# Optimization experiments

Hardware: AMD Instinct MI355X
Metric: run time of the kernel (lower is better)

The kernel has to match this reference:

```python
import jax, jax.numpy as jnp
import numpy as np

EPS = 1e-9
NUM_HEADS = 16
D = 1024      # input_dim == hidden_dim
B, S = 2, 2048


def layer_norm(x, scale, shift):
    mu = x.mean(axis=-1, keepdims=True)
    # torch std is unbiased (ddof=1); eps added to std, not variance
    std = jnp.std(x, axis=-1, ddof=1, keepdims=True)
    return scale * (x - mu) / (std + EPS) + shift


def setup_inputs() -> dict:
    key = jax.random.key(0)
    ks = jax.random.split(key, 18)
    d, h = D, D
    w = lambda k, sh: jax.random.normal(k, sh, dtype=jnp.float32) * 0.02
    return {
        "inputs": jax.random.normal(ks[0], (B, S, d), dtype=jnp.float32),
        "ln1_scale": jax.random.normal(ks[1], (d,), dtype=jnp.float32),
        "ln1_shift": jax.random.normal(ks[2], (d,), dtype=jnp.float32),
        "Wq": w(ks[3], (d, h)), "bq": jnp.zeros((h,), jnp.float32),
        "Wk": w(ks[4], (d, h)), "bk": jnp.zeros((h,), jnp.float32),
        "Wv": w(ks[5], (d, h)), "bv": jnp.zeros((h,), jnp.float32),
        "Wo": w(ks[6], (h, d)), "bo": jnp.zeros((d,), jnp.float32),
        "W1": w(ks[7], (d, 4 * d)), "b1": jnp.zeros((4 * d,), jnp.float32),
        "W2": w(ks[8], (4 * d, d)), "b2": jnp.zeros((d,), jnp.float32),
        "ln2_scale": jax.random.normal(ks[9], (d,), dtype=jnp.float32),
        "ln2_shift": jax.random.normal(ks[10], (d,), dtype=jnp.float32),
    }


def mhsa(x, Wq, bq, Wk, bk, Wv, bv, Wo, bo):
    b, s, d = x.shape
    nh, dh = NUM_HEADS, D // NUM_HEADS
    q = (x @ Wq + bq).reshape(b, s, nh, dh).transpose(0, 2, 1, 3)  # b h s d
    k = (x @ Wk + bk).reshape(b, s, nh, dh).transpose(0, 2, 1, 3)
    v = (x @ Wv + bv).reshape(b, s, nh, dh).transpose(0, 2, 1, 3)
    scores = jnp.einsum("bhqd,bhkd->bhqk", q, k) / jnp.sqrt(jnp.float32(dh))
    causal = jnp.triu(jnp.ones((s, s), dtype=bool), k=1)  # mask above diagonal
    scores = jnp.where(causal, -jnp.inf, scores)
    p = jax.nn.softmax(scores, axis=-1)
    p = jnp.where(jnp.isnan(p), 0.0, p)  # NaN-fill as in original
    out = jnp.einsum("bhqk,bhkd->bhqd", p, v)
    out = out.transpose(0, 2, 1, 3).reshape(b, s, nh * dh)
    return out @ Wo + bo


def reference(inputs, ln1_scale, ln1_shift, Wq, bq, Wk, bk, Wv, bv, Wo, bo,
              W1, b1, W2, b2, ln2_scale, ln2_shift):
    o1 = layer_norm(inputs, ln1_scale, ln1_shift)
    o1 = mhsa(o1, Wq, bq, Wk, bk, Wv, bv, Wo, bo) + inputs
    o2 = layer_norm(o1, ln2_scale, ln2_shift)
    # NOTE: original adds the residual from the *normalized* tensor, not o1
    ffn = jax.nn.relu(o2 @ W1 + b1) @ W2 + b2
    return ffn + o2
```

## Files before the change

### kernel.cpp

```cpp
#include <hip/hip_runtime.h>
#include <hip/hip_bf16.h>
#include <math.h>

#define BB 2
#define SS 2048
#define DD 1024
#define HH 16
#define DH 64
#define NROW (BB*SS)
#define FFN (4*DD)

typedef __attribute__((ext_vector_type(8))) __bf16 bf16x8;
typedef __attribute__((ext_vector_type(4))) __bf16 bf16x4;
typedef __attribute__((ext_vector_type(4))) float f32x4;

#define QSCALE 0.18033688011112042f

__device__ __forceinline__ ushort f2b(float f) {
    union { float f; uint32_t u; } x; x.f = f;
    uint32_t r = x.u + 0x7FFF + ((x.u >> 16) & 1);
    return (ushort)(r >> 16);
}
__device__ __forceinline__ float b2f(ushort u) {
    union { uint32_t u; float f; } x; x.u = (uint32_t)u << 16;
    return x.f;
}

__global__ __launch_bounds__(256)
void ln_kernel(const float* __restrict__ x, const float* __restrict__ scale,
               const float* __restrict__ shift, ushort* __restrict__ y) {
    int row = blockIdx.x;
    const float* xr = x + (size_t)row * DD;
    ushort* yr = y + (size_t)row * DD;
    int t = threadIdx.x;
    float v[4];
    float s = 0.f, ss = 0.f;
#pragma unroll
    for (int i = 0; i < 4; ++i) {
        v[i] = xr[t + 256 * i];
        s += v[i];
        ss += v[i] * v[i];
    }
#pragma unroll
    for (int off = 32; off; off >>= 1) {
        s  += __shfl_xor(s, off);
        ss += __shfl_xor(ss, off);
    }
    __shared__ float red[8];
    int w = t >> 6;
    if ((t & 63) == 0) { red[w] = s; red[w + 4] = ss; }
    __syncthreads();
    float st  = red[0] + red[1] + red[2] + red[3];
    float sst = red[4] + red[5] + red[6] + red[7];
    float mu = st * (1.f / DD);
    float var = (sst - DD * mu * mu) * (1.f / (DD - 1));
    var = fmaxf(var, 0.f);
    float inv = 1.f / (sqrtf(var) + 1e-9f);
#pragma unroll
    for (int i = 0; i < 4; ++i) {
        int c = t + 256 * i;
        yr[c] = f2b(scale[c] * (v[i] - mu) * inv + shift[c]);
    }
}

__global__ __launch_bounds__(256)
void ln_res_kernel(const ushort* __restrict__ xa, const float* __restrict__ xb,
                   const float* __restrict__ scale, const float* __restrict__ shift,
                   ushort* __restrict__ yb) {
    int row = blockIdx.x;
    const ushort* ar = xa + (size_t)row * DD;
    const float* br = xb + (size_t)row * DD;
    ushort* ybr = yb + (size_t)row * DD;
    int t = threadIdx.x;
    float v[4];
    float s = 0.f, ss = 0.f;
#pragma unroll
    for (int i = 0; i < 4; ++i) {
        int c = t + 256 * i;
        v[i] = b2f(ar[c]) + br[c];
        s += v[i];
        ss += v[i] * v[i];
    }
#pragma unroll
    for (int off = 32; off; off >>= 1) {
        s  += __shfl_xor(s, off);
        ss += __shfl_xor(ss, off);
    }
    __shared__ float red[8];
    int w = t >> 6;
    if ((t & 63) == 0) { red[w] = s; red[w + 4] = ss; }
    __syncthreads();
    float st  = red[0] + red[1] + red[2] + red[3];
    float sst = red[4] + red[5] + red[6] + red[7];
    float mu = st * (1.f / DD);
    float var = (sst - DD * mu * mu) * (1.f / (DD - 1));
    var = fmaxf(var, 0.f);
    float inv = 1.f / (sqrtf(var) + 1e-9f);
#pragma unroll
    for (int i = 0; i < 4; ++i) {
        int c = t + 256 * i;
        ybr[c] = f2b(scale[c] * (v[i] - mu) * inv + shift[c]);
    }
}

__global__ __launch_bounds__(256)
void transpose_bf16_kernel(const float* __restrict__ W, ushort* __restrict__ Wt,
                           int K, int N) {
    __shared__ ushort tile[32][33];
    int tx = threadIdx.x & 31;
    int ty = threadIdx.x >> 5;
    int n0 = blockIdx.x * 32;
    int k0 = blockIdx.y * 32;
#pragma unroll
    for (int i = 0; i < 32; i += 8)
        tile[ty + i][tx] = f2b(W[(size_t)(k0 + ty + i) * N + n0 + tx]);
    __syncthreads();
#pragma unroll
    for (int i = 0; i < 32; i += 8)
        Wt[(size_t)(n0 + ty + i) * K + k0 + tx] = tile[tx][ty + i];
}

__global__ __launch_bounds__(256)
void transpose4_bf16_kernel(const float* __restrict__ W0, const float* __restrict__ W1,
                            const float* __restrict__ W2, const float* __restrict__ W3,
                            ushort* __restrict__ Wt) {
    __shared__ ushort tile[32][33];
    int z = blockIdx.z;
    const float* W = z == 0 ? W0 : (z == 1 ? W1 : (z == 2 ? W2 : W3));
    ushort* dst = Wt + (size_t)z * DD * DD;
    int tx = threadIdx.x & 31;
    int ty = threadIdx.x >> 5;
    int n0 = blockIdx.x * 32;
    int k0 = blockIdx.y * 32;
#pragma unroll
    for (int i = 0; i < 32; i += 8)
        tile[ty + i][tx] = f2b(W[(size_t)(k0 + ty + i) * DD + n0 + tx]);
    __syncthreads();
#pragma unroll
    for (int i = 0; i < 32; i += 8)
        dst[(size_t)(n0 + ty + i) * DD + k0 + tx] = tile[tx][ty + i];
}

__global__ __launch_bounds__(256)
void reduce_wo_kernel(const float* __restrict__ p0, const float* __restrict__ p1,
                      const float* __restrict__ bias, ushort* __restrict__ yb) {
    int i = (blockIdx.x * 256 + threadIdx.x) * 4;
    float4 a = *reinterpret_cast<const float4*>(p0 + i);
    float4 b = *reinterpret_cast<const float4*>(p1 + i);
    int c = i & (DD - 1);
    float4 bs = *reinterpret_cast<const float4*>(bias + c);
    ushort4 o;
    o.x = f2b(a.x + b.x + bs.x);
    o.y = f2b(a.y + b.y + bs.y);
    o.z = f2b(a.z + b.z + bs.z);
    o.w = f2b(a.w + b.w + bs.w);
    *reinterpret_cast<ushort4*>(yb + i) = o;
}

__global__ __launch_bounds__(256)
void reduce_ffn2_kernel(const float* __restrict__ p0, const float* __restrict__ p1,
                        const float* __restrict__ bias, const ushort* __restrict__ res,
                        float* __restrict__ out) {
    int i = (blockIdx.x * 256 + threadIdx.x) * 4;
    float4 a = *reinterpret_cast<const float4*>(p0 + i);
    float4 b = *reinterpret_cast<const float4*>(p1 + i);
    ushort4 r = *reinterpret_cast<const ushort4*>(res + i);
    int c = i & (DD - 1);
    float4 bs = *reinterpret_cast<const float4*>(bias + c);
    float4 o;
    o.x = a.x + b.x + bs.x + b2f(r.x);
    o.y = a.y + b.y + bs.y + b2f(r.y);
    o.z = a.z + b.z + bs.z + b2f(r.z);
    o.w = a.w + b.w + bs.w + b2f(r.w);
    *reinterpret_cast<float4*>(out + i) = o;
}

#define GBM 128
#define GBK 32

template <int MODE, bool BF16_OUT, int DEPTH, int BN>
__global__ __launch_bounds__(512)
void gemm_bf16_kernel(const ushort* __restrict__ A, const ushort* __restrict__ Wt,
                      const float* __restrict__ bias, const ushort* __restrict__ addsrc,
                      void* __restrict__ Cout, int M, int N, int K, int lda,
                      const float* __restrict__ bias2, const float* __restrict__ bias3,
                      void* __restrict__ out2, void* __restrict__ out3) {
    __shared__ ushort As[DEPTH][GBM * GBK];
    __shared__ ushort Bs[DEPTH][BN * GBK];
    constexpr int NF = BN / 64;

    int tid = threadIdx.x;
    int lane = tid & 63;
    int wid = tid >> 6;
    int wr = wid >> 2, wc = wid & 3;

    int gx = gridDim.x;
    int nwg = gx * gridDim.y;
    int orig = blockIdx.y * gx + blockIdx.x;
    int q8 = nwg >> 3;
    int swz = (orig & 7) * q8 + (orig >> 3);
    int bx = swz % gx, by = swz / gx;

    int brow = by * GBM;
    int bcol = bx * BN;
    size_t koff = (size_t)blockIdx.z * K;

    int lrow = lane & 15;
    int kgrp = lane >> 4;

    f32x4 acc[4][NF] = {};

    auto stage = [&](int buf, int k0) {
        {
            int row = tid >> 2;
            int gran = (tid & 3) ^ ((row >> 1) & 3);
            const char* ga = (const char*)A +
                ((size_t)(brow + row) * lda + koff + k0) * 2 + gran * 16;
            __builtin_amdgcn_global_load_lds(
                (const __attribute__((address_space(1))) uint32_t*)ga,
                (__attribute__((address_space(3))) uint32_t*)(&As[buf][0] + (wid * 16) * GBK),
                16, 0, 0);
        }
#pragma unroll
        for (int i = 0; i < BN / 128; ++i) {
            int idx = i * 512 + tid;
            int row = idx >> 2;
            int gran = (idx & 3) ^ ((row >> 1) & 3);
            const char* gb = (const char*)Wt +
                ((size_t)(bcol + row) * lda + koff + k0) * 2 + gran * 16;
            __builtin_amdgcn_global_load_lds(
                (const __attribute__((address_space(1))) uint32_t*)gb,
                (__attribute__((address_space(3))) uint32_t*)(&Bs[buf][0] + (i * 128 + wid * 16) * GBK),
                16, 0, 0);
        }
    };

    int nk = K / GBK;
    constexpr int PRE = DEPTH - 1;
#pragma unroll
    for (int s = 0; s < PRE; ++s)
        if (s < nk) stage(s, s * GBK);

    int cur = 0, stg = PRE;
    for (int t = 0; t < nk; ++t) {
        __builtin_amdgcn_sched_barrier(0);
        int rem = nk - 1 - t;
        if constexpr (DEPTH == 5 && BN == 128) {
            if (rem >= 3)      asm volatile("s_waitcnt vmcnt(6)" ::: "memory");
            else if (rem == 2) asm volatile("s_waitcnt vmcnt(4)" ::: "memory");
            else if (rem == 1) asm volatile("s_waitcnt vmcnt(2)" ::: "memory");
            else               asm volatile("s_waitcnt vmcnt(0)" ::: "memory");
        } else if constexpr (DEPTH == 3 && BN == 128) {
            if (rem >= 1)      asm volatile("s_waitcnt vmcnt(2)" ::: "memory");
            else               asm volatile("s_waitcnt vmcnt(0)" ::: "memory");
        } else if constexpr (DEPTH == 3 && BN == 256) {
            if (rem >= 1)      asm volatile("s_waitcnt vmcnt(3)" ::: "memory");
            else               asm volatile("s_waitcnt vmcnt(0)" ::: "memory");
        } else {
            asm volatile("s_waitcnt vmcnt(0)" ::: "memory");
        }
        asm volatile("s_barrier" ::: "memory");
        if (t + PRE < nk) stage(stg, (t + PRE) * GBK);

        bf16x8 afrag[4], bfrag[NF];
#pragma unroll
        for (int mi = 0; mi < 4; ++mi) {
            int row = wr * 64 + mi * 16 + lrow;
            int gran = kgrp ^ ((row >> 1) & 3);
            afrag[mi] = *(const bf16x8*)((const char*)&As[cur][0] + row * 64 + gran * 16);
        }
#pragma unroll
        for (int ni = 0; ni < NF; ++ni) {
            int row = wc * (BN / 4) + ni * 16 + lrow;
            int gran = kgrp ^ ((row >> 1) & 3);
            bfrag[ni] = *(const bf16x8*)((const char*)&Bs[cur][0] + row * 64 + gran * 16);
        }
#pragma unroll
        for (int mi = 0; mi < 4; ++mi)
#pragma unroll
            for (int ni = 0; ni < NF; ++ni)
                acc[mi][ni] = __builtin_amdgcn_mfma_f32_16x16x32_bf16(
                    afrag[mi], bfrag[ni], acc[mi][ni], 0, 0, 0);

        cur = (cur == DEPTH - 1) ? 0 : cur + 1;
        stg = (stg == DEPTH - 1) ? 0 : stg + 1;
    }

    if (MODE == 3) {
        int which = bcol >> 10;
        const float* bs = which == 0 ? bias : (which == 1 ? bias2 : bias3);
#pragma unroll
        for (int ni = 0; ni < NF; ++ni) {
            int col = bcol + wc * (BN / 4) + ni * 16 + lrow;
            int lcol = col & 1023;
            float bsv = bs[lcol];
#pragma unroll
            for (int mi = 0; mi < 4; ++mi) {
                f32x4 a = acc[mi][ni];
#pragma unroll
                for (int j = 0; j < 4; ++j) {
                    int row = brow + wr * 64 + mi * 16 + kgrp * 4 + j;
                    float val = a[j] + bsv;
                    if (which == 2) {
                        size_t idx = (size_t)(row >> 11) * ((size_t)DD * SS)
                                   + (size_t)lcol * SS + (row & (SS - 1));
                        ((ushort*)out3)[idx] = f2b(val);
                    } else if (which == 0) {
                        ((ushort*)Cout)[(size_t)row * DD + lcol] = f2b(val * QSCALE);
                    } else {
                        ((ushort*)out2)[(size_t)row * DD + lcol] = f2b(val);
                    }
                }
            }
        }
        return;
    }

    if (MODE == 4) {
        float* dst = (float*)Cout + (size_t)blockIdx.z * ((size_t)M * N);
#pragma unroll
        for (int ni = 0; ni < NF; ++ni) {
            int col = bcol + wc * (BN / 4) + ni * 16 + lrow;
#pragma unroll
            for (int mi = 0; mi < 4; ++mi) {
                f32x4 a = acc[mi][ni];
#pragma unroll
                for (int j = 0; j < 4; ++j) {
                    int row = brow + wr * 64 + mi * 16 + kgrp * 4 + j;
                    dst[(size_t)row * N + col] = a[j];
                }
            }
        }
        return;
    }

#pragma unroll
    for (int ni = 0; ni < NF; ++ni) {
        int col = bcol + wc * (BN / 4) + ni * 16 + lrow;
        float bsv = bias[col];
#pragma unroll
        for (int mi = 0; mi < 4; ++mi) {
            f32x4 a = acc[mi][ni];
#pragma unroll
            for (int j = 0; j < 4; ++j) {
                int row = brow + wr * 64 + mi * 16 + kgrp * 4 + j;
                float val = a[j] + bsv;
                if (MODE == 1) val = fmaxf(val, 0.f);
                if (BF16_OUT)
                    ((ushort*)Cout)[(size_t)row * N + col] = f2b(val);
                else
                    ((float*)Cout)[(size_t)row * N + col] = val;
            }
        }
    }
}

__global__ __launch_bounds__(256)
void attn_mfma_kernel(const ushort* __restrict__ Qg, const ushort* __restrict__ Kg,
                      const ushort* __restrict__ Vtg, ushort* __restrict__ Og) {
    __shared__ ushort Qs[64 * 64];
    __shared__ ushort Ks[2][64 * 64];
    __shared__ ushort Vs[2][64 * 64];

    int tid = threadIdx.x;
    int lane = tid & 63;
    int wid = tid >> 6;
    int bh = blockIdx.x;
    int b = bh >> 4, h = bh & 15;
    int y = blockIdx.y;
    int jj = y >> 3, kk = y & 7;
    int qt = jj * 8 + ((jj & 1) ? 7 - kk : kk);
    int q0 = qt * 64;

    const ushort* Qbase = Qg + ((size_t)(b * SS + q0)) * DD + h * DH;
    const ushort* Kbase = Kg + ((size_t)(b * SS)) * DD + h * DH;
    const ushort* Vbase = Vtg + (size_t)bh * DH * SS;

    int r0 = wid * 16;
    int rr0 = r0 + (lane >> 3);
    int g0 = lane & 7;
    int g = lane >> 4;
    int lr = lane & 15;

    auto stageKV = [&](int buf, int k0) {
#pragma unroll
        for (int i = 0; i < 2; ++i) {
            int rr = rr0 + i * 8;
            int gg = g0 ^ (rr & 7);
            const ushort* srck = Kbase + (size_t)(k0 + rr) * DD + gg * 8;
            __builtin_amdgcn_global_load_lds(
                (const __attribute__((address_space(1))) uint32_t*)srck,
                (__attribute__((address_space(3))) uint32_t*)(&Ks[buf][0] + (r0 + i * 8) * 64),
                16, 0, 0);
            const ushort* srcv = Vbase + (size_t)rr * SS + k0 + gg * 8;
            __builtin_amdgcn_global_load_lds(
                (const __attribute__((address_space(1))) uint32_t*)srcv,
                (__attribute__((address_space(3))) uint32_t*)(&Vs[buf][0] + (r0 + i * 8) * 64),
                16, 0, 0);
        }
    };

    int nt = q0 / 64 + 1;

    {
#pragma unroll
        for (int i = 0; i < 2; ++i) {
            int rr = rr0 + i * 8;
            int gg = g0 ^ (rr & 7);
            const ushort* src = Qbase + (size_t)rr * DD + gg * 8;
            __builtin_amdgcn_global_load_lds(
                (const __attribute__((address_space(1))) uint32_t*)src,
                (__attribute__((address_space(3))) uint32_t*)(Qs + (r0 + i * 8) * 64),
                16, 0, 0);
        }
    }
    stageKV(0, 0);
    asm volatile("s_waitcnt vmcnt(4)" ::: "memory");

    bf16x8 aq[2];
    {
        int r = wid * 16 + lr;
#pragma unroll
        for (int ks = 0; ks < 2; ++ks) {
            int lg = ks * 4 + g;
            aq[ks] = *(const bf16x8*)((const char*)Qs + r * 128 + ((lg ^ (r & 7)) << 4));
        }
    }
    ushort* Ps = Qs;

    f32x4 oacc[4] = {};
    float m = -INFINITY, l = 0.f;
    const float THR = 11.0f;
    int qa = q0 + wid * 16 + lr;

    int cur = 0;
    for (int t = 0; t < nt; ++t) {
        __builtin_amdgcn_sched_barrier(0);
        asm volatile("s_waitcnt vmcnt(0)" ::: "memory");
        asm volatile("s_barrier" ::: "memory");
        if (t + 1 < nt) stageKV(cur ^ 1, (t + 1) * 64);
        int k0 = t * 64;

        f32x4 sacc[4] = {};
        __builtin_amdgcn_s_setprio(1);
#pragma unroll
        for (int ni = 0; ni < 4; ++ni) {
            int r = ni * 16 + lr;
#pragma unroll
            for (int ks = 0; ks < 2; ++ks) {
                int lg = ks * 4 + g;
                bf16x8 bk = *(const bf16x8*)((const char*)&Ks[cur][0] + r * 128 + ((lg ^ (r & 7)) << 4));
                sacc[ni] = __builtin_amdgcn_mfma_f32_16x16x32_bf16(bk, aq[ks], sacc[ni], 0, 0, 0);
            }
        }
        __builtin_amdgcn_s_setprio(0);

        if (k0 == q0) {
#pragma unroll
            for (int ni = 0; ni < 4; ++ni) {
#pragma unroll
                for (int j = 0; j < 4; ++j) {
                    int key = q0 + ni * 16 + g * 4 + j;
                    if (key > qa) sacc[ni][j] = -INFINITY;
                }
            }
        }

        float mx = sacc[0][0];
#pragma unroll
        for (int ni = 0; ni < 4; ++ni)
#pragma unroll
            for (int j = 0; j < 4; ++j) mx = fmaxf(mx, sacc[ni][j]);
        mx = fmaxf(mx, __shfl_xor(mx, 16));
        mx = fmaxf(mx, __shfl_xor(mx, 32));

        if (__any(mx > m + THR)) {
            float mn = fmaxf(m, mx);
            float corr = __builtin_amdgcn_exp2f(m - mn);
            m = mn;
            l *= corr;
            float cj[4];
#pragma unroll
            for (int j = 0; j < 4; ++j)
                cj[j] = __shfl(corr, (lane & 48) | (g * 4 + j));
#pragma unroll
            for (int ni = 0; ni < 4; ++ni)
#pragma unroll
                for (int j = 0; j < 4; ++j) oacc[ni][j] *= cj[j];
        }

        float p[4][4];
        float rs = 0.f;
#pragma unroll
        for (int ni = 0; ni < 4; ++ni)
#pragma unroll
            for (int j = 0; j < 4; ++j) {
                p[ni][j] = __builtin_amdgcn_exp2f(sacc[ni][j] - m);
                rs += p[ni][j];
            }
        rs += __shfl_xor(rs, 16);
        rs += __shfl_xor(rs, 32);
        l += rs;

        {
            int row = wid * 16 + lr;
#pragma unroll
            for (int ni = 0; ni < 4; ++ni) {
                bf16x4 w4 = { (__bf16)p[ni][0], (__bf16)p[ni][1],
                              (__bf16)p[ni][2], (__bf16)p[ni][3] };
                int gran = (ni * 2 + (g >> 1)) ^ (row & 7);
                *(bf16x4*)((char*)Ps + row * 128 + (gran << 4) + (g & 1) * 8) = w4;
            }
        }
        asm volatile("s_waitcnt lgkmcnt(0)" ::: "memory");

        bf16x8 ap[2];
        {
            int r = wid * 16 + lr;
#pragma unroll
            for (int ks = 0; ks < 2; ++ks) {
                int lg = ks * 4 + g;
                ap[ks] = *(const bf16x8*)((const char*)Ps + r * 128 + ((lg ^ (r & 7)) << 4));
            }
        }
        __builtin_amdgcn_s_setprio(1);
#pragma unroll
        for (int ni = 0; ni < 4; ++ni) {
            int r = ni * 16 + lr;
#pragma unroll
            for (int ks = 0; ks < 2; ++ks) {
                int lg = ks * 4 + g;
                bf16x8 bv = *(const bf16x8*)((const char*)&Vs[cur][0] + r * 128 + ((lg ^ (r & 7)) << 4));
                oacc[ni] = __builtin_amdgcn_mfma_f32_16x16x32_bf16(ap[ks], bv, oacc[ni], 0, 0, 0);
            }
        }
        __builtin_amdgcn_s_setprio(0);
        cur ^= 1;
    }

#pragma unroll
    for (int j = 0; j < 4; ++j) {
        float lj = __shfl(l, (lane & 48) | (g * 4 + j));
        float inv = 1.f / lj;
        int gr = q0 + wid * 16 + g * 4 + j;
#pragma unroll
        for (int ni = 0; ni < 4; ++ni) {
            int d = ni * 16 + lr;
            Og[((size_t)(b * SS + gr)) * DD + h * DH + d] = f2b(oacc[ni][j] * inv);
        }
    }
}

extern "C" void kernel_launch(void* const* d_in, const int* in_sizes, int n_in,
                              void* d_out, int out_size, void* d_ws, size_t ws_size,
                              hipStream_t stream) {
    const float* inputs    = (const float*)d_in[0];
    const float* ln1_scale = (const float*)d_in[1];
    const float* ln1_shift = (const float*)d_in[2];
    const float* Wq = (const float*)d_in[3];
    const float* bq = (const float*)d_in[4];
    const float* Wk = (const float*)d_in[5];
    const float* bk = (const float*)d_in[6];
    const float* Wv = (const float*)d_in[7];
    const float* bv = (const float*)d_in[8];
    const float* Wo = (const float*)d_in[9];
    const float* bo = (const float*)d_in[10];
    const float* W1 = (const float*)d_in[11];
    const float* b1 = (const float*)d_in[12];
    const float* W2 = (const float*)d_in[13];
    const float* b2 = (const float*)d_in[14];
    const float* ln2_scale = (const float*)d_in[15];
    const float* ln2_shift = (const float*)d_in[16];
    float* out = (float*)d_out;

    const size_t MB = 1024 * 1024;
    char* w = (char*)d_ws;
    ushort* q_b   = (ushort*)(w + 0 * MB);
    ushort* k_b   = (ushort*)(w + 8 * MB);
    ushort* vt_b  = (ushort*)(w + 16 * MB);
    ushort* att_b = (ushort*)(w + 24 * MB);
    float*  pw    = (float*)(w + 32 * MB);
    ushort* proj_b= (ushort*)(w + 0 * MB);
    ushort* o2_b  = (ushort*)(w + 8 * MB);
    float*  pf    = (float*)(w + 16 * MB);
    ushort* h1_b  = (ushort*)(w + 64 * MB);
    ushort* wq_t  = (ushort*)(w + 96 * MB);
    ushort* wk_t  = (ushort*)(w + 98 * MB);
    ushort* wv_t  = (ushort*)(w + 100 * MB);
    ushort* wo_t  = (ushort*)(w + 102 * MB);
    ushort* w1_t  = (ushort*)(w + 104 * MB);
    ushort* w2_t  = (ushort*)(w + 112 * MB);
    ushort* xn_b  = (ushort*)(w + 120 * MB);

    transpose4_bf16_kernel<<<dim3(DD / 32, DD / 32, 4), 256, 0, stream>>>(
        Wq, Wk, Wv, Wo, wq_t);
    transpose_bf16_kernel<<<dim3(FFN / 32, DD / 32), 256, 0, stream>>>(W1, w1_t, DD, FFN);
    transpose_bf16_kernel<<<dim3(DD / 32, FFN / 32), 256, 0, stream>>>(W2, w2_t, FFN, DD);

    ln_kernel<<<NROW, 256, 0, stream>>>(inputs, ln1_scale, ln1_shift, xn_b);

    dim3 gqkv(3 * DD / 128, NROW / GBM, 1);
    gemm_bf16_kernel<3, true, 3, 128><<<gqkv, 512, 0, stream>>>(
        xn_b, wq_t, bq, nullptr, q_b, NROW, 3 * DD, DD, DD, bk, bv, k_b, vt_b);

    dim3 ga(BB * HH, SS / 64);
    attn_mfma_kernel<<<ga, 256, 0, stream>>>(q_b, k_b, vt_b, att_b);

    dim3 g1z(DD / 128, NROW / GBM, 2);
    gemm_bf16_kernel<4, false, 5, 128><<<g1z, 512, 0, stream>>>(
        att_b, wo_t, nullptr, nullptr, pw, NROW, DD, DD / 2, DD, nullptr, nullptr, nullptr, nullptr);
    reduce_wo_kernel<<<(NROW * DD / 4) / 256, 256, 0, stream>>>(
        pw, pw + (size_t)NROW * DD, bo, proj_b);

    ln_res_kernel<<<NROW, 256, 0, stream>>>(proj_b, inputs, ln2_scale, ln2_shift, o2_b);

    dim3 g2(FFN / 256, NROW / GBM, 1);
    gemm_bf16_kernel<1, true, 3, 256><<<g2, 512, 0, stream>>>(
        o2_b, w1_t, b1, nullptr, h1_b, NROW, FFN, DD, DD, nullptr, nullptr, nullptr, nullptr);

    gemm_bf16_kernel<4, false, 5, 128><<<g1z, 512, 0, stream>>>(
        h1_b, w2_t, nullptr, nullptr, pf, NROW, DD, FFN / 2, FFN, nullptr, nullptr, nullptr, nullptr);
    reduce_ffn2_kernel<<<(NROW * DD / 4) / 256, 256, 0, stream>>>(
        pf, pf + (size_t)NROW * DD, b2, o2_b, out);
}
```

Baseline: 237.1 us.

## Use 4-way split-K with bf16 partials and wider tiles for Wo/FFN2 GEMMs

The Wo and FFN2 GEMMs move from 2-way split-K with 128-wide N tiles and fp32 partial outputs to 4-way split-K with 256-wide N tiles and bf16 partial outputs. The reduce kernels now sum four bf16 partials in float before adding bias and residual. The aim is to cut partial-sum write and read traffic and to change tile shape and pipeline depth for better reuse. The grid keeps the same block count, and each partial is rounded to bf16, which adds some accuracy loss.

```diff
diff --git a/kernel.cpp b/kernel.cpp
--- a/kernel.cpp
+++ b/kernel.cpp
@@ -142,36 +142,41 @@
 }
 
 __global__ __launch_bounds__(256)
-void reduce_wo_kernel(const float* __restrict__ p0, const float* __restrict__ p1,
-                      const float* __restrict__ bias, ushort* __restrict__ yb) {
+void reduce_wo_kernel(const ushort* __restrict__ p, const float* __restrict__ bias,
+                      ushort* __restrict__ yb) {
+    const size_t MN = (size_t)NROW * DD;
     int i = (blockIdx.x * 256 + threadIdx.x) * 4;
-    float4 a = *reinterpret_cast<const float4*>(p0 + i);
-    float4 b = *reinterpret_cast<const float4*>(p1 + i);
+    ushort4 a = *reinterpret_cast<const ushort4*>(p + i);
+    ushort4 b = *reinterpret_cast<const ushort4*>(p + MN + i);
+    ushort4 c4 = *reinterpret_cast<const ushort4*>(p + 2 * MN + i);
+    ushort4 d4 = *reinterpret_cast<const ushort4*>(p + 3 * MN + i);
     int c = i & (DD - 1);
     float4 bs = *reinterpret_cast<const float4*>(bias + c);
     ushort4 o;
-    o.x = f2b(a.x + b.x + bs.x);
-    o.y = f2b(a.y + b.y + bs.y);
-    o.z = f2b(a.z + b.z + bs.z);
-    o.w = f2b(a.w + b.w + bs.w);
+    o.x = f2b(b2f(a.x) + b2f(b.x) + b2f(c4.x) + b2f(d4.x) + bs.x);
+    o.y = f2b(b2f(a.y) + b2f(b.y) + b2f(c4.y) + b2f(d4.y) + bs.y);
+    o.z = f2b(b2f(a.z) + b2f(b.z) + b2f(c4.z) + b2f(d4.z) + bs.z);
+    o.w = f2b(b2f(a.w) + b2f(b.w) + b2f(c4.w) + b2f(d4.w) + bs.w);
     *reinterpret_cast<ushort4*>(yb + i) = o;
 }
 
 __global__ __launch_bounds__(256)
-void reduce_ffn2_kernel(const float* __restrict__ p0, const float* __restrict__ p1,
-                        const float* __restrict__ bias, const ushort* __restrict__ res,
-                        float* __restrict__ out) {
+void reduce_ffn2_kernel(const ushort* __restrict__ p, const float* __restrict__ bias,
+                        const ushort* __restrict__ res, float* __restrict__ out) {
+    const size_t MN = (size_t)NROW * DD;
     int i = (blockIdx.x * 256 + threadIdx.x) * 4;
-    float4 a = *reinterpret_cast<const float4*>(p0 + i);
-    float4 b = *reinterpret_cast<const float4*>(p1 + i);
+    ushort4 a = *reinterpret_cast<const ushort4*>(p + i);
+    ushort4 b = *reinterpret_cast<const ushort4*>(p + MN + i);
+    ushort4 c4 = *reinterpret_cast<const ushort4*>(p + 2 * MN + i);
+    ushort4 d4 = *reinterpret_cast<const ushort4*>(p + 3 * MN + i);
     ushort4 r = *reinterpret_cast<const ushort4*>(res + i);
     int c = i & (DD - 1);
     float4 bs = *reinterpret_cast<const float4*>(bias + c);
     float4 o;
-    o.x = a.x + b.x + bs.x + b2f(r.x);
-    o.y = a.y + b.y + bs.y + b2f(r.y);
-    o.z = a.z + b.z + bs.z + b2f(r.z);
-    o.w = a.w + b.w + bs.w + b2f(r.w);
+    o.x = b2f(a.x) + b2f(b.x) + b2f(c4.x) + b2f(d4.x) + bs.x + b2f(r.x);
+    o.y = b2f(a.y) + b2f(b.y) + b2f(c4.y) + b2f(d4.y) + bs.y + b2f(r.y);
+    o.z = b2f(a.z) + b2f(b.z) + b2f(c4.z) + b2f(d4.z) + bs.z + b2f(r.z);
+    o.w = b2f(a.w) + b2f(b.w) + b2f(c4.w) + b2f(d4.w) + bs.w + b2f(r.w);
     *reinterpret_cast<float4*>(out + i) = o;
 }
 
@@ -317,7 +322,7 @@
     }
 
     if (MODE == 4) {
-        float* dst = (float*)Cout + (size_t)blockIdx.z * ((size_t)M * N);
+        ushort* dst = (ushort*)Cout + (size_t)blockIdx.z * ((size_t)M * N);
 #pragma unroll
         for (int ni = 0; ni < NF; ++ni) {
             int col = bcol + wc * (BN / 4) + ni * 16 + lrow;
@@ -327,7 +332,7 @@
 #pragma unroll
                 for (int j = 0; j < 4; ++j) {
                     int row = brow + wr * 64 + mi * 16 + kgrp * 4 + j;
-                    dst[(size_t)row * N + col] = a[j];
+                    dst[(size_t)row * N + col] = f2b(a[j]);
                 }
             }
         }
@@ -579,10 +584,10 @@
     ushort* k_b   = (ushort*)(w + 8 * MB);
     ushort* vt_b  = (ushort*)(w + 16 * MB);
     ushort* att_b = (ushort*)(w + 24 * MB);
-    float*  pw    = (float*)(w + 32 * MB);
+    ushort* pw    = (ushort*)(w + 32 * MB);
     ushort* proj_b= (ushort*)(w + 0 * MB);
     ushort* o2_b  = (ushort*)(w + 8 * MB);
-    float*  pf    = (float*)(w + 16 * MB);
+    ushort* pf    = (ushort*)(w + 16 * MB);
     ushort* h1_b  = (ushort*)(w + 64 * MB);
     ushort* wq_t  = (ushort*)(w + 96 * MB);
     ushort* wk_t  = (ushort*)(w + 98 * MB);
@@ -606,11 +611,10 @@
     dim3 ga(BB * HH, SS / 64);
     attn_mfma_kernel<<<ga, 256, 0, stream>>>(q_b, k_b, vt_b, att_b);
 
-    dim3 g1z(DD / 128, NROW / GBM, 2);
-    gemm_bf16_kernel<4, false, 5, 128><<<g1z, 512, 0, stream>>>(
-        att_b, wo_t, nullptr, nullptr, pw, NROW, DD, DD / 2, DD, nullptr, nullptr, nullptr, nullptr);
-    reduce_wo_kernel<<<(NROW * DD / 4) / 256, 256, 0, stream>>>(
-        pw, pw + (size_t)NROW * DD, bo, proj_b);
+    dim3 gwo(DD / 256, NROW / GBM, 4);
+    gemm_bf16_kernel<4, false, 3, 256><<<gwo, 512, 0, stream>>>(
+        att_b, wo_t, nullptr, nullptr, pw, NROW, DD, DD / 4, DD, nullptr, nullptr, nullptr, nullptr);
+    reduce_wo_kernel<<<(NROW * DD / 4) / 256, 256, 0, stream>>>(pw, bo, proj_b);
 
     ln_res_kernel<<<NROW, 256, 0, stream>>>(proj_b, inputs, ln2_scale, ln2_shift, o2_b);
 
@@ -618,8 +622,8 @@
     gemm_bf16_kernel<1, true, 3, 256><<<g2, 512, 0, stream>>>(
         o2_b, w1_t, b1, nullptr, h1_b, NROW, FFN, DD, DD, nullptr, nullptr, nullptr, nullptr);
 
-    gemm_bf16_kernel<4, false, 5, 128><<<g1z, 512, 0, stream>>>(
-        h1_b, w2_t, nullptr, nullptr, pf, NROW, DD, FFN / 2, FFN, nullptr, nullptr, nullptr, nullptr);
-    reduce_ffn2_kernel<<<(NROW * DD / 4) / 256, 256, 0, stream>>>(
-        pf, pf + (size_t)NROW * DD, b2, o2_b, out);
-}
+    dim3 gf2(DD / 256, NROW / GBM, 4);
+    gemm_bf16_kernel<4, false, 3, 256><<<gf2, 512, 0, stream>>>(
+        h1_b, w2_t, nullptr, nullptr, pf, NROW, DD, FFN / 4, FFN, nullptr, nullptr, nullptr, nullptr);
+    reduce_ffn2_kernel<<<(NROW * DD / 4) / 256, 256, 0, stream>>>(pf, b2, o2_b, out);
+}
```

New measurement: 231.7 us. -2.3%, faster.
